# Kernel optimization log

Hardware: AMD Instinct MI355X
Metric: run time of the kernel (lower is better)

## Reference

```python
import jax, jax.numpy as jnp
import numpy as np

N = 50000   # nodes
E = 800000  # edges
F = 256     # in_channels
H = 256     # hidden (GCN output)


def setup_inputs() -> dict:
    key = jax.random.key(0)
    ks = jax.random.split(key, 6)
    x = jax.random.normal(ks[0], (N, F), jnp.float32)
    edge_index = jax.random.randint(ks[1], (2, E), 0, N)
    perm = jax.random.permutation(ks[2], N)
    W = jax.random.normal(ks[3], (F, H), jnp.float32) / np.sqrt(F)
    b = jnp.zeros((H,), jnp.float32)
    a = jnp.full((1,), 0.25, jnp.float32)  # PReLU slope
    disc_W = jax.random.normal(ks[4], (H, H), jnp.float32) / np.sqrt(H)
    return {"x": x, "W": W, "b": b, "a": a, "disc_W": disc_W,
            "edge_index": edge_index, "perm": perm}


def _gcn(x, W, b, src, dst, n):
    # GCNConv: linear -> symmetric-normalized aggregation (with self-loops) -> bias
    xw = x @ W  # [N, H]
    loop = jnp.arange(n)
    s = jnp.concatenate([src, loop])
    d = jnp.concatenate([dst, loop])
    ew = jnp.ones(s.shape[0], xw.dtype)
    deg = jax.ops.segment_sum(ew, d, num_segments=n)          # [N]
    dinv = jnp.where(deg > 0, jax.lax.rsqrt(deg), 0.0)
    norm = dinv[s] * dinv[d]                                   # [E+N]
    out = jax.ops.segment_sum(xw[s] * norm[:, None], d, num_segments=n)
    return out + b


def reference(x, W, b, a, disc_W, edge_index, perm):
    src, dst = edge_index[0], edge_index[1]
    n = x.shape[0]

    def encode(feat):
        h = _gcn(feat, W, b, src, dst, n)
        return jnp.where(h >= 0, h, a * h)  # PReLU

    z1 = encode(x)          # clean
    z2 = encode(x[perm])    # corrupted (row permutation)
    summary = jax.nn.sigmoid(z1.mean(axis=0))  # [H]
    wsum = disc_W @ summary                     # [H]
    pos = z1 @ wsum  # [N]
    neg = z2 @ wsum  # [N]
    return pos, neg
```

## Files before the change

### kernel.cpp

```cpp
#include <hip/hip_runtime.h>

#define N_NODES 50000
#define N_EDGES 800000
#define DIM 256
#define NB 196
#define UNROLL 8
#define MAXE (N_EDGES + N_NODES * UNROLL)
#define CSB 512
#define NCH 4
#define CCOLS 64
#define CHSZ (N_NODES * CCOLS)
#define RPB 16
#define CHB (N_NODES / RPB)

typedef __attribute__((ext_vector_type(8))) short bf16x8;
typedef __attribute__((ext_vector_type(4))) float f32x4;
typedef __attribute__((ext_vector_type(2))) float f32x2;

__device__ __forceinline__ unsigned int f2bf(float f) {
  unsigned int u = __float_as_uint(f);
  return (u + 0x7FFFu + ((u >> 16) & 1u)) >> 16;
}
__device__ __forceinline__ float bf_lo(unsigned int u) {
  return __uint_as_float(u << 16);
}
__device__ __forceinline__ float bf_hi(unsigned int u) {
  return __uint_as_float(u & 0xFFFF0000u);
}


__global__ void k_deg(const int* __restrict__ dst, int* __restrict__ deg) {
  int e = blockIdx.x * blockDim.x + threadIdx.x;
  if (e < N_EDGES) atomicAdd(&deg[dst[e]], 1);
}

__global__ __launch_bounds__(256) void k_alloc(const int* __restrict__ deg,
                                               float* __restrict__ dinv,
                                               int* __restrict__ gcur,
                                               int2* __restrict__ rse,
                                               int* __restrict__ cursor) {
  __shared__ int s[256];
  __shared__ int base;
  const int t = threadIdx.x;
  const int i = blockIdx.x * 256 + t;
  int d = 0, pd = 0;
  if (i < N_NODES) {
    d = deg[i];
    dinv[i] = rsqrtf((float)(d + 1));
    pd = (d + UNROLL - 1) & ~(UNROLL - 1);
  }
  s[t] = pd;
  __syncthreads();
  for (int off = 1; off < 256; off <<= 1) {
    int u = (t >= off) ? s[t - off] : 0;
    __syncthreads();
    s[t] += u;
    __syncthreads();
  }
  if (t == 255) base = atomicAdd(gcur, s[255]);
  __syncthreads();
  if (i < N_NODES) {
    int rs = base + s[t] - pd;
    rse[i] = make_int2(rs, rs + pd);
    cursor[i] = rs;
  }
}

__global__ void k_scatter(const int* __restrict__ src, const int* __restrict__ dst,
                          const int* __restrict__ perm, const float* __restrict__ dinv,
                          int* __restrict__ cursor, uint2* __restrict__ meta) {
  int e = blockIdx.x * blockDim.x + threadIdx.x;
  if (e < N_EDGES) {
    int s = src[e], d = dst[e];
    int p = atomicAdd(&cursor[d], 1);
    meta[p] = make_uint2((unsigned)s | ((unsigned)perm[s] << 16),
                         __float_as_uint(dinv[s] * dinv[d]));
  }
}


__global__ void k_prep(const float* __restrict__ W, ushort* __restrict__ Wt) {
  int n = blockIdx.x, k = threadIdx.x;
  Wt[n * DIM + k] = (ushort)f2bf(W[k * DIM + n]);
}


__global__ __launch_bounds__(256) void k_gemm(const float* __restrict__ X,
                                              const ushort* __restrict__ Wt,
                                              ushort* __restrict__ XWC) {
  __shared__ ushort Xs[64 * 40];
  __shared__ ushort Ws[256 * 40];
  const int tid = threadIdx.x;
  const int lane = tid & 63;
  const int w = tid >> 6;
  const int m0 = blockIdx.x * 64;
  const int l16 = lane & 15, kh = lane >> 4;

  f32x4 acc[4][4];
#pragma unroll
  for (int mf = 0; mf < 4; ++mf)
#pragma unroll
    for (int nf = 0; nf < 4; ++nf) acc[mf][nf] = (f32x4){0.f, 0.f, 0.f, 0.f};

  for (int k0 = 0; k0 < DIM; k0 += 32) {
#pragma unroll
    for (int it = 0; it < 2; ++it) {
      int idx = tid + it * 256;
      int row = idx >> 3, q = idx & 7;
      int grow = m0 + row;
      float4 v = make_float4(0.f, 0.f, 0.f, 0.f);
      if (grow < N_NODES)
        v = *reinterpret_cast<const float4*>(&X[(size_t)grow * DIM + k0 + q * 4]);
      uint2 p;
      p.x = f2bf(v.x) | (f2bf(v.y) << 16);
      p.y = f2bf(v.z) | (f2bf(v.w) << 16);
      *reinterpret_cast<uint2*>(&Xs[row * 40 + q * 4]) = p;
    }
#pragma unroll
    for (int it = 0; it < 4; ++it) {
      int idx = tid + it * 256;
      int n = idx >> 2, c = idx & 3;
      uint4 wv = *reinterpret_cast<const uint4*>(&Wt[n * DIM + k0 + c * 8]);
      *reinterpret_cast<uint4*>(&Ws[n * 40 + c * 8]) = wv;
    }
    __syncthreads();
    bf16x8 a[4], b[4];
#pragma unroll
    for (int f = 0; f < 4; ++f) {
      a[f] = *reinterpret_cast<const bf16x8*>(&Ws[(w * 64 + f * 16 + l16) * 40 + kh * 8]);
      b[f] = *reinterpret_cast<const bf16x8*>(&Xs[(f * 16 + l16) * 40 + kh * 8]);
    }
#pragma unroll
    for (int mf = 0; mf < 4; ++mf)
#pragma unroll
      for (int nf = 0; nf < 4; ++nf)
        acc[mf][nf] = __builtin_amdgcn_mfma_f32_16x16x32_bf16(a[nf], b[mf],
                                                              acc[mf][nf], 0, 0, 0);
    __syncthreads();
  }
#pragma unroll
  for (int mf = 0; mf < 4; ++mf) {
    int m = m0 + mf * 16 + l16;
    if (m >= N_NODES) continue;
#pragma unroll
    for (int nf = 0; nf < 4; ++nf) {
      int cb = nf * 16 + kh * 4;
      uint2 p;
      p.x = f2bf(acc[mf][nf][0]) | (f2bf(acc[mf][nf][1]) << 16);
      p.y = f2bf(acc[mf][nf][2]) | (f2bf(acc[mf][nf][3]) << 16);
      *reinterpret_cast<uint2*>(&XWC[(size_t)w * CHSZ + (size_t)m * CCOLS + cb]) = p;
    }
  }
}


__device__ __forceinline__ void fma8v(f32x2* A, uint4 v, f32x2 n) {
  A[0] += (f32x2){bf_lo(v.x), bf_hi(v.x)} * n;
  A[1] += (f32x2){bf_lo(v.y), bf_hi(v.y)} * n;
  A[2] += (f32x2){bf_lo(v.z), bf_hi(v.z)} * n;
  A[3] += (f32x2){bf_lo(v.w), bf_hi(v.w)} * n;
}

__global__ __launch_bounds__(256) void k_aggc(
    const ushort* __restrict__ xwc, const int2* __restrict__ rse,
    const uint2* __restrict__ meta, const int* __restrict__ perm,
    const float* __restrict__ dinv, const float* __restrict__ bias,
    const float* __restrict__ slope, ushort* __restrict__ z1,
    ushort* __restrict__ z2) {
  const int blk = blockIdx.x;
  const int ch = blk / CHB;
  const int rb = blk % CHB;
  const int tid = threadIdx.x;
  const int r = rb * RPB + (tid >> 4);
  const int l = tid & 15;
  const int eg = l >> 3;
  const int sc = l & 7;
  const ushort* xc = xwc + (size_t)ch * CHSZ;
  const ushort* xcs = xc + sc * 8;

  f32x2 a1[4] = {{0.f, 0.f}, {0.f, 0.f}, {0.f, 0.f}, {0.f, 0.f}};
  f32x2 a2[4] = {{0.f, 0.f}, {0.f, 0.f}, {0.f, 0.f}, {0.f, 0.f}};
  const int2 se = rse[r];
  for (int e = se.x; e < se.y; e += 8) {
    uint4 m0 = *reinterpret_cast<const uint4*>(meta + e + eg * 2);
    uint4 m1 = *reinterpret_cast<const uint4*>(meta + e + 4 + eg * 2);
    uint4 vA1 = *reinterpret_cast<const uint4*>(xcs + ((m0.x & 0xFFFFu) << 6));
    uint4 vA2 = *reinterpret_cast<const uint4*>(xcs + ((m0.x >> 16) << 6));
    uint4 vB1 = *reinterpret_cast<const uint4*>(xcs + ((m0.z & 0xFFFFu) << 6));
    uint4 vB2 = *reinterpret_cast<const uint4*>(xcs + ((m0.z >> 16) << 6));
    uint4 vC1 = *reinterpret_cast<const uint4*>(xcs + ((m1.x & 0xFFFFu) << 6));
    uint4 vC2 = *reinterpret_cast<const uint4*>(xcs + ((m1.x >> 16) << 6));
    uint4 vD1 = *reinterpret_cast<const uint4*>(xcs + ((m1.z & 0xFFFFu) << 6));
    uint4 vD2 = *reinterpret_cast<const uint4*>(xcs + ((m1.z >> 16) << 6));
    const float fA = __uint_as_float(m0.y), fB = __uint_as_float(m0.w);
    const float fC = __uint_as_float(m1.y), fD = __uint_as_float(m1.w);
    const f32x2 nA = {fA, fA}, nB = {fB, fB}, nC = {fC, fC}, nD = {fD, fD};
    fma8v(a1, vA1, nA); fma8v(a2, vA2, nA);
    fma8v(a1, vB1, nB); fma8v(a2, vB2, nB);
    fma8v(a1, vC1, nC); fma8v(a2, vC2, nC);
    fma8v(a1, vD1, nD); fma8v(a2, vD2, nD);
  }
#pragma unroll
  for (int j = 0; j < 4; ++j) {
    a1[j].x += __shfl_xor(a1[j].x, 8);
    a1[j].y += __shfl_xor(a1[j].y, 8);
    a2[j].x += __shfl_xor(a2[j].x, 8);
    a2[j].y += __shfl_xor(a2[j].y, 8);
  }
  if (eg == 0) {
    const float di = dinv[r];
    const float d2 = di * di;
    const f32x2 nd = {d2, d2};
    const int pr = perm[r];
    uint4 s1 = *reinterpret_cast<const uint4*>(xcs + ((unsigned)r << 6));
    uint4 s2 = *reinterpret_cast<const uint4*>(xcs + ((unsigned)pr << 6));
    fma8v(a1, s1, nd); fma8v(a2, s2, nd);
    const float* bp = bias + ch * CCOLS + sc * 8;
    float4 b0 = *reinterpret_cast<const float4*>(bp);
    float4 b1 = *reinterpret_cast<const float4*>(bp + 4);
    a1[0] += (f32x2){b0.x, b0.y}; a1[1] += (f32x2){b0.z, b0.w};
    a1[2] += (f32x2){b1.x, b1.y}; a1[3] += (f32x2){b1.z, b1.w};
    a2[0] += (f32x2){b0.x, b0.y}; a2[1] += (f32x2){b0.z, b0.w};
    a2[2] += (f32x2){b1.x, b1.y}; a2[3] += (f32x2){b1.z, b1.w};
    const float a0 = slope[0];
#pragma unroll
    for (int j = 0; j < 4; ++j) {
      a1[j].x = a1[j].x >= 0.f ? a1[j].x : a0 * a1[j].x;
      a1[j].y = a1[j].y >= 0.f ? a1[j].y : a0 * a1[j].y;
      a2[j].x = a2[j].x >= 0.f ? a2[j].x : a0 * a2[j].x;
      a2[j].y = a2[j].y >= 0.f ? a2[j].y : a0 * a2[j].y;
    }
    uint4 p1, p2;
    p1.x = f2bf(a1[0].x) | (f2bf(a1[0].y) << 16);
    p1.y = f2bf(a1[1].x) | (f2bf(a1[1].y) << 16);
    p1.z = f2bf(a1[2].x) | (f2bf(a1[2].y) << 16);
    p1.w = f2bf(a1[3].x) | (f2bf(a1[3].y) << 16);
    p2.x = f2bf(a2[0].x) | (f2bf(a2[0].y) << 16);
    p2.y = f2bf(a2[1].x) | (f2bf(a2[1].y) << 16);
    p2.z = f2bf(a2[2].x) | (f2bf(a2[2].y) << 16);
    p2.w = f2bf(a2[3].x) | (f2bf(a2[3].y) << 16);
    const size_t o = (size_t)r * DIM + ch * CCOLS + sc * 8;
    *reinterpret_cast<uint4*>(z1 + o) = p1;
    *reinterpret_cast<uint4*>(z2 + o) = p2;
  }
}


__global__ __launch_bounds__(256) void k_colsum(const ushort* __restrict__ z1,
                                                float* __restrict__ partial) {
  __shared__ float red[8 * 256];
  const int t = threadIdx.x;
  const int c8 = t & 31;
  const int g = t >> 5;
  float s[8] = {0.f, 0.f, 0.f, 0.f, 0.f, 0.f, 0.f, 0.f};
  for (int r = blockIdx.x * 8 + g; r < N_NODES; r += 8 * CSB) {
    uint4 v = *reinterpret_cast<const uint4*>(z1 + (size_t)r * DIM + c8 * 8);
    s[0] += bf_lo(v.x); s[1] += bf_hi(v.x);
    s[2] += bf_lo(v.y); s[3] += bf_hi(v.y);
    s[4] += bf_lo(v.z); s[5] += bf_hi(v.z);
    s[6] += bf_lo(v.w); s[7] += bf_hi(v.w);
  }
#pragma unroll
  for (int j = 0; j < 8; ++j) red[g * 256 + c8 * 8 + j] = s[j];
  __syncthreads();
  float tot = 0.f;
#pragma unroll
  for (int g2 = 0; g2 < 8; ++g2) tot += red[g2 * 256 + t];
  partial[blockIdx.x * 256 + t] = tot;
}

__global__ __launch_bounds__(256) void k_wsum(const float* __restrict__ partial,
                                              const float* __restrict__ disc_W,
                                              float* __restrict__ wsum) {
  __shared__ float s[DIM];
  const int t = threadIdx.x;
  float a0 = 0.f, a1 = 0.f, a2 = 0.f, a3 = 0.f;
  for (int b = 0; b < CSB; b += 4) {
    a0 += partial[(b + 0) * 256 + t];
    a1 += partial[(b + 1) * 256 + t];
    a2 += partial[(b + 2) * 256 + t];
    a3 += partial[(b + 3) * 256 + t];
  }
  float m = (a0 + a1 + a2 + a3) * (1.0f / (float)N_NODES);
  s[t] = 1.0f / (1.0f + expf(-m));
  __syncthreads();
  float acc = 0.f;
  for (int j = 0; j < DIM; j += 4) {
    float4 w4 = *reinterpret_cast<const float4*>(&disc_W[t * DIM + j]);
    acc += w4.x * s[j] + w4.y * s[j + 1] + w4.z * s[j + 2] + w4.w * s[j + 3];
  }
  wsum[t] = acc;
}


__global__ __launch_bounds__(256) void k_posneg(const ushort* __restrict__ z1,
                                                const ushort* __restrict__ z2,
                                                const float* __restrict__ wsum,
                                                float* __restrict__ pos,
                                                float* __restrict__ neg) {
  const int wid = (blockIdx.x * blockDim.x + threadIdx.x) >> 6;
  const int lane = threadIdx.x & 63;
  if (wid >= N_NODES) return;
  uint2 v1 = *reinterpret_cast<const uint2*>(z1 + (size_t)wid * DIM + lane * 4);
  uint2 v2 = *reinterpret_cast<const uint2*>(z2 + (size_t)wid * DIM + lane * 4);
  float4 w4 = *reinterpret_cast<const float4*>(&wsum[lane * 4]);
  float dp = bf_lo(v1.x) * w4.x + bf_hi(v1.x) * w4.y + bf_lo(v1.y) * w4.z + bf_hi(v1.y) * w4.w;
  float dn = bf_lo(v2.x) * w4.x + bf_hi(v2.x) * w4.y + bf_lo(v2.y) * w4.z + bf_hi(v2.y) * w4.w;
#pragma unroll
  for (int off = 32; off > 0; off >>= 1) {
    dp += __shfl_down(dp, off);
    dn += __shfl_down(dn, off);
  }
  if (lane == 0) { pos[wid] = dp; neg[wid] = dn; }
}


extern "C" void kernel_launch(void* const* d_in, const int* in_sizes, int n_in,
                              void* d_out, int out_size, void* d_ws, size_t ws_size,
                              hipStream_t stream) {
  const float* x      = (const float*)d_in[0];
  const float* W      = (const float*)d_in[1];
  const float* b      = (const float*)d_in[2];
  const float* a      = (const float*)d_in[3];
  const float* disc_W = (const float*)d_in[4];
  const int*   eidx   = (const int*)d_in[5];
  const int*   perm   = (const int*)d_in[6];
  const int* src = eidx;
  const int* dst = eidx + N_EDGES;

  constexpr size_t SZ_BFM  = (size_t)N_NODES * DIM * 2;
  constexpr size_t SZ_META = (size_t)MAXE * 8;
  constexpr size_t OFF_XWC = 0;
  constexpr size_t OFF_Z1  = OFF_XWC + SZ_BFM;
  constexpr size_t OFF_Z2  = OFF_Z1 + SZ_BFM;
  constexpr size_t OFF_WT  = OFF_Z2 + SZ_BFM;
  constexpr size_t OFF_DEG = OFF_WT + 131072;
  constexpr size_t OFF_GC  = OFF_DEG + 200000;
  constexpr size_t OFF_DNV = OFF_DEG + 200192;
  constexpr size_t OFF_RSE = OFF_DNV + 200192;
  constexpr size_t OFF_CUR = OFF_RSE + 400128;
  constexpr size_t OFF_MT  = OFF_CUR + 200192;
  constexpr size_t OFF_WSM = OFF_MT + SZ_META;
  constexpr size_t OFF_PT  = OFF_WSM + 1024;
  constexpr size_t NEED    = OFF_PT + (size_t)CSB * 256 * 4;
  if (ws_size < NEED) return;

  char* ws = (char*)d_ws;
  ushort* xwc    = (ushort*)(ws + OFF_XWC);
  ushort* z1     = (ushort*)(ws + OFF_Z1);
  ushort* z2     = (ushort*)(ws + OFF_Z2);
  ushort* Wt     = (ushort*)(ws + OFF_WT);
  int*    deg    = (int*)(ws + OFF_DEG);
  int*    gcur   = (int*)(ws + OFF_GC);
  float*  dinv   = (float*)(ws + OFF_DNV);
  int2*   rse    = (int2*)(ws + OFF_RSE);
  int*    cursor = (int*)(ws + OFF_CUR);
  uint2*  meta   = (uint2*)(ws + OFF_MT);
  float*  wsum   = (float*)(ws + OFF_WSM);
  float*  partial= (float*)(ws + OFF_PT);

  float* pos = (float*)d_out;
  float* neg = pos + N_NODES;

  hipMemsetAsync(deg, 0, 200064, stream);
  hipMemsetAsync(meta, 0, SZ_META, stream);

  k_deg<<<(N_EDGES + 255) / 256, 256, 0, stream>>>(dst, deg);
  k_alloc<<<NB, 256, 0, stream>>>(deg, dinv, gcur, rse, cursor);
  k_scatter<<<(N_EDGES + 255) / 256, 256, 0, stream>>>(src, dst, perm, dinv,
                                                       cursor, meta);

  k_prep<<<DIM, DIM, 0, stream>>>(W, Wt);
  k_gemm<<<(N_NODES + 63) / 64, 256, 0, stream>>>(x, Wt, xwc);

  k_aggc<<<NCH * CHB, 256, 0, stream>>>(xwc, rse, meta, perm, dinv, b, a, z1, z2);

  k_colsum<<<CSB, 256, 0, stream>>>(z1, partial);
  k_wsum<<<1, 256, 0, stream>>>(partial, disc_W, wsum);
  k_posneg<<<(N_NODES * 64 + 255) / 256, 256, 0, stream>>>(z1, z2, wsum, pos, neg);
}
```

Before: 240.2 us.

## Sort rows by padded degree for balanced aggregation and drop full meta memset

```diff
diff --git a/kernel.cpp b/kernel.cpp
--- a/kernel.cpp
+++ b/kernel.cpp
@@ -6,12 +6,13 @@
 #define NB 196
 #define UNROLL 8
 #define MAXE (N_EDGES + N_NODES * UNROLL)
-#define CSB 512
+#define CSB 256
 #define NCH 4
 #define CCOLS 64
 #define CHSZ (N_NODES * CCOLS)
 #define RPB 16
 #define CHB (N_NODES / RPB)
+#define NBIN 32
 
 typedef __attribute__((ext_vector_type(8))) short bf16x8;
 typedef __attribute__((ext_vector_type(4))) float f32x4;
@@ -37,12 +38,16 @@
 __global__ __launch_bounds__(256) void k_alloc(const int* __restrict__ deg,
                                                float* __restrict__ dinv,
                                                int* __restrict__ gcur,
+                                               int* __restrict__ bincnt,
                                                int2* __restrict__ rse,
-                                               int* __restrict__ cursor) {
+                                               int* __restrict__ cursor,
+                                               uint2* __restrict__ meta) {
   __shared__ int s[256];
   __shared__ int base;
+  __shared__ int lbin[NBIN];
   const int t = threadIdx.x;
   const int i = blockIdx.x * 256 + t;
+  if (t < NBIN) lbin[t] = 0;
   int d = 0, pd = 0;
   if (i < N_NODES) {
     d = deg[i];
@@ -58,12 +63,44 @@
     __syncthreads();
   }
   if (t == 255) base = atomicAdd(gcur, s[255]);
-  __syncthreads();
+  if (i < N_NODES) atomicAdd(&lbin[min(pd >> 3, NBIN - 1)], 1);
+  __syncthreads();
+  if (t < NBIN && lbin[t]) atomicAdd(&bincnt[t], lbin[t]);
   if (i < N_NODES) {
     int rs = base + s[t] - pd;
     rse[i] = make_int2(rs, rs + pd);
     cursor[i] = rs;
-  }
+    for (int j = d; j < pd; ++j) meta[rs + j] = make_uint2(0u, 0u);
+  }
+}
+
+__global__ void k_binscan(const int* __restrict__ bincnt, int* __restrict__ bincur) {
+  if (threadIdx.x == 0) {
+    int run = 0;
+    for (int b = 0; b < NBIN; ++b) { bincur[b] = run; run += bincnt[b]; }
+  }
+}
+
+__global__ __launch_bounds__(256) void k_rank(const int* __restrict__ deg,
+                                              int* __restrict__ bincur,
+                                              int* __restrict__ order) {
+  __shared__ int lcnt[NBIN];
+  __shared__ int lbase[NBIN];
+  const int t = threadIdx.x;
+  const int i = blockIdx.x * 256 + t;
+  if (t < NBIN) lcnt[t] = 0;
+  __syncthreads();
+  int bin = 0, my = 0;
+  const bool ok = i < N_NODES;
+  if (ok) {
+    int pd = (deg[i] + UNROLL - 1) & ~(UNROLL - 1);
+    bin = min(pd >> 3, NBIN - 1);
+    my = atomicAdd(&lcnt[bin], 1);
+  }
+  __syncthreads();
+  if (t < NBIN && lcnt[t]) lbase[t] = atomicAdd(&bincur[t], lcnt[t]);
+  __syncthreads();
+  if (ok) order[lbase[bin] + my] = i;
 }
 
 __global__ void k_scatter(const int* __restrict__ src, const int* __restrict__ dst,
@@ -155,23 +192,23 @@
 
 
 __device__ __forceinline__ void fma8v(f32x2* A, uint4 v, f32x2 n) {
-  A[0] += (f32x2){bf_lo(v.x), bf_hi(v.x)} * n;
-  A[1] += (f32x2){bf_lo(v.y), bf_hi(v.y)} * n;
-  A[2] += (f32x2){bf_lo(v.z), bf_hi(v.z)} * n;
-  A[3] += (f32x2){bf_lo(v.w), bf_hi(v.w)} * n;
+  A[0] += (f32x2){__uint_as_float(v.x << 16), __uint_as_float(v.x)} * n;
+  A[1] += (f32x2){__uint_as_float(v.y << 16), __uint_as_float(v.y)} * n;
+  A[2] += (f32x2){__uint_as_float(v.z << 16), __uint_as_float(v.z)} * n;
+  A[3] += (f32x2){__uint_as_float(v.w << 16), __uint_as_float(v.w)} * n;
 }
 
 __global__ __launch_bounds__(256) void k_aggc(
     const ushort* __restrict__ xwc, const int2* __restrict__ rse,
-    const uint2* __restrict__ meta, const int* __restrict__ perm,
-    const float* __restrict__ dinv, const float* __restrict__ bias,
-    const float* __restrict__ slope, ushort* __restrict__ z1,
-    ushort* __restrict__ z2) {
+    const uint2* __restrict__ meta, const int* __restrict__ order,
+    const int* __restrict__ perm, const float* __restrict__ dinv,
+    const float* __restrict__ bias, const float* __restrict__ slope,
+    ushort* __restrict__ z1, ushort* __restrict__ z2) {
   const int blk = blockIdx.x;
   const int ch = blk / CHB;
   const int rb = blk % CHB;
   const int tid = threadIdx.x;
-  const int r = rb * RPB + (tid >> 4);
+  const int r = order[rb * RPB + (tid >> 4)];
   const int l = tid & 15;
   const int eg = l >> 3;
   const int sc = l & 7;
@@ -336,10 +373,14 @@
   constexpr size_t OFF_WT  = OFF_Z2 + SZ_BFM;
   constexpr size_t OFF_DEG = OFF_WT + 131072;
   constexpr size_t OFF_GC  = OFF_DEG + 200000;
-  constexpr size_t OFF_DNV = OFF_DEG + 200192;
+  constexpr size_t OFF_BC  = OFF_GC + 4;
+  constexpr size_t OFF_BU  = OFF_BC + 128;
+  constexpr size_t ZERO_SZ = 200000 + 4 + 128 + 128;
+  constexpr size_t OFF_DNV = OFF_DEG + 200448;
   constexpr size_t OFF_RSE = OFF_DNV + 200192;
   constexpr size_t OFF_CUR = OFF_RSE + 400128;
-  constexpr size_t OFF_MT  = OFF_CUR + 200192;
+  constexpr size_t OFF_ORD = OFF_CUR + 200192;
+  constexpr size_t OFF_MT  = OFF_ORD + 200192;
   constexpr size_t OFF_WSM = OFF_MT + SZ_META;
   constexpr size_t OFF_PT  = OFF_WSM + 1024;
   constexpr size_t NEED    = OFF_PT + (size_t)CSB * 256 * 4;
@@ -352,9 +393,12 @@
   ushort* Wt     = (ushort*)(ws + OFF_WT);
   int*    deg    = (int*)(ws + OFF_DEG);
   int*    gcur   = (int*)(ws + OFF_GC);
+  int*    bincnt = (int*)(ws + OFF_BC);
+  int*    bincur = (int*)(ws + OFF_BU);
   float*  dinv   = (float*)(ws + OFF_DNV);
   int2*   rse    = (int2*)(ws + OFF_RSE);
   int*    cursor = (int*)(ws + OFF_CUR);
+  int*    order  = (int*)(ws + OFF_ORD);
   uint2*  meta   = (uint2*)(ws + OFF_MT);
   float*  wsum   = (float*)(ws + OFF_WSM);
   float*  partial= (float*)(ws + OFF_PT);
@@ -362,18 +406,20 @@
   float* pos = (float*)d_out;
   float* neg = pos + N_NODES;
 
-  hipMemsetAsync(deg, 0, 200064, stream);
-  hipMemsetAsync(meta, 0, SZ_META, stream);
+  hipMemsetAsync(deg, 0, 200448, stream);
 
   k_deg<<<(N_EDGES + 255) / 256, 256, 0, stream>>>(dst, deg);
-  k_alloc<<<NB, 256, 0, stream>>>(deg, dinv, gcur, rse, cursor);
+  k_alloc<<<NB, 256, 0, stream>>>(deg, dinv, gcur, bincnt, rse, cursor, meta);
+  k_binscan<<<1, 64, 0, stream>>>(bincnt, bincur);
+  k_rank<<<NB, 256, 0, stream>>>(deg, bincur, order);
   k_scatter<<<(N_EDGES + 255) / 256, 256, 0, stream>>>(src, dst, perm, dinv,
                                                        cursor, meta);
 
   k_prep<<<DIM, DIM, 0, stream>>>(W, Wt);
   k_gemm<<<(N_NODES + 63) / 64, 256, 0, stream>>>(x, Wt, xwc);
 
-  k_aggc<<<NCH * CHB, 256, 0, stream>>>(xwc, rse, meta, perm, dinv, b, a, z1, z2);
+  k_aggc<<<NCH * CHB, 256, 0, stream>>>(xwc, rse, meta, order, perm, dinv,
+                                        b, a, z1, z2);
 
   k_colsum<<<CSB, 256, 0, stream>>>(z1, partial);
   k_wsum<<<1, 256, 0, stream>>>(partial, disc_W, wsum);
```

After: 242.8 us. About the same (+1.1%).
